# Kernel tuning notes

Measured on AMD Instinct MI355X. Metric: run time of the kernel, lower is better.

## Reference

```python
import jax, jax.numpy as jnp
import numpy as np

V, D = 100000, 300          # vocab, embedding dim
B, L, T, C, I = 64, 256, 1, 10, 6  # batch, positions, targets, context, info samples


def setup_inputs() -> dict:
    key = jax.random.key(0)
    ks = jax.random.split(key, 8)
    # indices start at 1 so padding_idx=0 (zero row, no grad in torch) never appears
    pos_u = jax.random.randint(ks[0], (B, L, T), 1, V)
    pos_v = jax.random.randint(ks[1], (B, L, C), 1, V)
    info_v = jax.random.randint(ks[2], (B, L, I), 1, V)
    initrange = 1.0 / D
    W_out = jax.random.uniform(ks[3], (V, D), minval=-initrange, maxval=initrange, dtype=jnp.float32)
    # torch inits W_in to 0; use a small random init so the baseline is non-degenerate
    W_in = jax.random.uniform(ks[4], (V, D), minval=-initrange, maxval=initrange, dtype=jnp.float32)
    W_out = W_out.at[0].set(0.0)
    W_in = W_in.at[0].set(0.0)
    context_mask = (jax.random.uniform(ks[5], (C,)) > 0.2).astype(jnp.float32)
    sig_mask = jnp.where(jax.random.uniform(ks[6], (I,)) > 0.5, 1.0, -1.0).astype(jnp.float32)
    score_mask = jax.random.uniform(ks[7], (I,), dtype=jnp.float32)
    return {"pos_u": pos_u, "pos_v": pos_v, "info_v": info_v,
            "W_in": W_in, "W_out": W_out,
            "context_mask": context_mask, "sig_mask": sig_mask, "score_mask": score_mask}


def reference(pos_u, pos_v, info_v, W_in, W_out, context_mask, sig_mask, score_mask):
    tgt_out = W_out[pos_u]    # [B,L,T,D]
    ctx_in = W_in[pos_v]      # [B,L,C,D]
    ctx_out = W_out[pos_v]    # [B,L,C,D]
    info_in = W_in[info_v]    # [B,L,I,D]
    # dropout disabled (p=0, eval-mode determinism)
    ctx_in = ctx_in * context_mask[None, None, :, None]
    # target-context scores: [B,L,T,C]
    score = jnp.einsum('bltd,blcd->bltc', tgt_out, ctx_in)
    score = jnp.clip(score, -10.0, 10.0)
    loss = -jnp.sum(jax.nn.log_sigmoid(score))
    # context-info scores: [B,L,C,I]
    info_score = jnp.einsum('blcd,blid->blci', ctx_out, info_in)
    info_score = jnp.clip(info_score, -10.0, 10.0)
    info_score = info_score * sig_mask          # sign flip for negative samples
    info_score = -jax.nn.log_sigmoid(info_score) * score_mask
    return loss + jnp.sum(info_score)
```

## Files before the change

### kernel.cpp

```cpp
#include <hip/hip_runtime.h>

#define D_ 300
#define C_ 10
#define I_ 6
#define NPOS 16384
#define PPB 4
#define NBLK (NPOS / PPB)
#define NDOT 70
#define RED_LD 71

__device__ __forceinline__ float neg_log_sigmoid(float x) {
    return __logf(1.0f + __expf(-x));
}

__device__ __forceinline__ float dot4(float4 a, float4 b) {
    return a.x * b.x + a.y * b.y + a.z * b.z + a.w * b.w;
}

__global__ __launch_bounds__(256, 4) void hg2vec_pos_kernel(
    const int* __restrict__ pos_u, const int* __restrict__ pos_v,
    const int* __restrict__ info_v,
    const float* __restrict__ W_in, const float* __restrict__ W_out,
    const float* __restrict__ context_mask, const float* __restrict__ sig_mask,
    const float* __restrict__ score_mask, float* __restrict__ partial)
{
    const int wave = threadIdx.x >> 6;
    const int lane = threadIdx.x & 63;
    const int p = blockIdx.x * PPB + wave;

    __shared__ float s_red[PPB][8][RED_LD];

    const int su = __builtin_amdgcn_readfirstlane(pos_u[p]);
    int scv[C_], siv[I_];
#pragma unroll
    for (int c = 0; c < C_; ++c) scv[c] = __builtin_amdgcn_readfirstlane(pos_v[p * C_ + c]);
#pragma unroll
    for (int i = 0; i < I_; ++i) siv[i] = __builtin_amdgcn_readfirstlane(info_v[p * I_ + i]);

    const int o0 = 4 * lane;
    const int l1 = (lane < 11) ? lane : 0;
    const int o1 = 256 + 4 * l1;
    const float zf = (lane < 11) ? 1.0f : 0.0f;

    const float* ur = W_out + (size_t)su * D_;
    float4 u0 = *(const float4*)(ur + o0);
    float4 u1 = *(const float4*)(ur + o1);
    u1.x *= zf; u1.y *= zf; u1.z *= zf; u1.w *= zf;

    float4 in0[I_], in1[I_];
#pragma unroll
    for (int i = 0; i < I_; ++i) {
        const float* r = W_in + (size_t)siv[i] * D_;
        in0[i] = *(const float4*)(r + o0);
        float4 t = *(const float4*)(r + o1);
        t.x *= zf; t.y *= zf; t.z *= zf; t.w *= zf;
        in1[i] = t;
    }

    const int g = lane >> 3;
    const bool writer = (lane & 7) == 0;

#pragma unroll
    for (int c = 0; c < C_; ++c) {
        const float* cir = W_in  + (size_t)scv[c] * D_;
        const float* cor = W_out + (size_t)scv[c] * D_;
        const float4 a0 = *(const float4*)(cir + o0);
        const float4 a1 = *(const float4*)(cir + o1);
        const float4 b0 = *(const float4*)(cor + o0);
        const float4 b1 = *(const float4*)(cor + o1);

        float part[7];
        part[0] = dot4(u0, a0) + dot4(u1, a1);
#pragma unroll
        for (int i = 0; i < I_; ++i)
            part[1 + i] = dot4(b0, in0[i]) + dot4(b1, in1[i]);

#pragma unroll
        for (int t = 0; t < 7; ++t) {
            float v = part[t];
            v += __shfl_xor(v, 1, 64);
            v += __shfl_xor(v, 2, 64);
            v += __shfl_xor(v, 4, 64);
            if (writer) s_red[wave][g][c * 7 + t] = v;
        }
    }

    float acc = 0.0f;
#pragma unroll
    for (int pass = 0; pass < 2; ++pass) {
        const int d = pass * 64 + lane;
        if (d < NDOT) {
            float s = s_red[wave][0][d] + s_red[wave][1][d] + s_red[wave][2][d]
                    + s_red[wave][3][d] + s_red[wave][4][d] + s_red[wave][5][d]
                    + s_red[wave][6][d] + s_red[wave][7][d];
            const int c = d / 7;
            const int t = d - c * 7;
            if (t == 0) {
                float x = s * context_mask[c];
                x = fminf(fmaxf(x, -10.0f), 10.0f);
                acc += neg_log_sigmoid(x);
            } else {
                const int i = t - 1;
                float x = fminf(fmaxf(s, -10.0f), 10.0f) * sig_mask[i];
                acc += neg_log_sigmoid(x) * score_mask[i];
            }
        }
    }

#pragma unroll
    for (int off = 32; off; off >>= 1) acc += __shfl_xor(acc, off, 64);
    if (lane == 0) partial[p] = acc;
}

__global__ __launch_bounds__(256) void hg2vec_reduce_kernel(
    const float* __restrict__ partial, float* __restrict__ out)
{
    float a = 0.0f;
    const float4* p4 = (const float4*)partial;
    for (int i = threadIdx.x; i < NPOS / 4; i += 256) {
        float4 v = p4[i];
        a += (v.x + v.y) + (v.z + v.w);
    }
#pragma unroll
    for (int off = 32; off; off >>= 1) a += __shfl_xor(a, off, 64);
    __shared__ float s[4];
    if ((threadIdx.x & 63) == 0) s[threadIdx.x >> 6] = a;
    __syncthreads();
    if (threadIdx.x == 0) out[0] = (s[0] + s[1]) + (s[2] + s[3]);
}

extern "C" void kernel_launch(void* const* d_in, const int* in_sizes, int n_in,
                              void* d_out, int out_size, void* d_ws, size_t ws_size,
                              hipStream_t stream) {
    const int* pos_u = (const int*)d_in[0];
    const int* pos_v = (const int*)d_in[1];
    const int* info_v = (const int*)d_in[2];
    const float* W_in = (const float*)d_in[3];
    const float* W_out = (const float*)d_in[4];
    const float* context_mask = (const float*)d_in[5];
    const float* sig_mask = (const float*)d_in[6];
    const float* score_mask = (const float*)d_in[7];
    float* out = (float*)d_out;
    float* partial = (float*)d_ws;

    hg2vec_pos_kernel<<<NBLK, 256, 0, stream>>>(
        pos_u, pos_v, info_v, W_in, W_out,
        context_mask, sig_mask, score_mask, partial);
    hg2vec_reduce_kernel<<<1, 256, 0, stream>>>(partial, out);
}
```

Baseline: 300.9 us.

## Double-buffer gathered embedding rows into LDS with async global_load_lds per wave

```diff
diff --git a/kernel.cpp b/kernel.cpp
--- a/kernel.cpp
+++ b/kernel.cpp
@@ -4,129 +4,176 @@
 #define C_ 10
 #define I_ 6
 #define NPOS 16384
-#define PPB 4
-#define NBLK (NPOS / PPB)
+#define NROWS 27
 #define NDOT 70
-#define RED_LD 71
+#define ROWF 304
+#define BUFPAD 212
+#define BUFF (NROWS * ROWF + BUFPAD)
+#define WPB 2
+#define PPW 32
+#define NBLK (NPOS / (WPB * PPW))
+#define NPART (NBLK * WPB)
 
 __device__ __forceinline__ float neg_log_sigmoid(float x) {
     return __logf(1.0f + __expf(-x));
 }
-
 __device__ __forceinline__ float dot4(float4 a, float4 b) {
     return a.x * b.x + a.y * b.y + a.z * b.z + a.w * b.w;
 }
+__device__ __forceinline__ void dma16(const float* g, float* l) {
+    __builtin_amdgcn_global_load_lds(
+        (const __attribute__((address_space(1))) void*)g,
+        (__attribute__((address_space(3))) void*)l, 16, 0, 0);
+}
 
-__global__ __launch_bounds__(256, 4) void hg2vec_pos_kernel(
+__global__ __launch_bounds__(128) void hg2vec_pos_kernel(
     const int* __restrict__ pos_u, const int* __restrict__ pos_v,
     const int* __restrict__ info_v,
     const float* __restrict__ W_in, const float* __restrict__ W_out,
     const float* __restrict__ context_mask, const float* __restrict__ sig_mask,
     const float* __restrict__ score_mask, float* __restrict__ partial)
 {
-    const int wave = threadIdx.x >> 6;
+    const int wv = __builtin_amdgcn_readfirstlane((int)(threadIdx.x >> 6));
     const int lane = threadIdx.x & 63;
-    const int p = blockIdx.x * PPB + wave;
+    const int p0 = (blockIdx.x * WPB + wv) * PPW;
 
-    __shared__ float s_red[PPB][8][RED_LD];
+    __shared__ float s_buf[WPB][2][BUFF];
+    __shared__ float s_red[WPB][8][71];
 
-    const int su = __builtin_amdgcn_readfirstlane(pos_u[p]);
-    int scv[C_], siv[I_];
-#pragma unroll
-    for (int c = 0; c < C_; ++c) scv[c] = __builtin_amdgcn_readfirstlane(pos_v[p * C_ + c]);
-#pragma unroll
-    for (int i = 0; i < I_; ++i) siv[i] = __builtin_amdgcn_readfirstlane(info_v[p * I_ + i]);
+    const int d1 = lane;
+    const int c1 = d1 / 7, t1 = d1 - 7 * c1;
+    float m1_cm = 0, m1_sm = 0, m1_scm = 0;
+    if (t1 == 0) m1_cm = context_mask[c1];
+    else { m1_sm = sig_mask[t1 - 1]; m1_scm = score_mask[t1 - 1]; }
+    const int d2 = 64 + lane;
+    const bool has2 = d2 < NDOT;
+    const int c2 = d2 / 7, t2 = d2 - 7 * c2;
+    float m2_sm = 0, m2_scm = 0;
+    if (has2) { m2_sm = sig_mask[t2 - 1]; m2_scm = score_mask[t2 - 1]; }
 
-    const int o0 = 4 * lane;
-    const int l1 = (lane < 11) ? lane : 0;
-    const int o1 = 256 + 4 * l1;
+    const int lc = (lane < 11) ? lane : 10;
     const float zf = (lane < 11) ? 1.0f : 0.0f;
 
-    const float* ur = W_out + (size_t)su * D_;
-    float4 u0 = *(const float4*)(ur + o0);
-    float4 u1 = *(const float4*)(ur + o1);
-    u1.x *= zf; u1.y *= zf; u1.z *= zf; u1.w *= zf;
-
-    float4 in0[I_], in1[I_];
+    int su, scv[C_], siv[I_];
+    auto load_idx = [&](int p) {
+        su = pos_u[p];
 #pragma unroll
-    for (int i = 0; i < I_; ++i) {
-        const float* r = W_in + (size_t)siv[i] * D_;
-        in0[i] = *(const float4*)(r + o0);
-        float4 t = *(const float4*)(r + o1);
-        t.x *= zf; t.y *= zf; t.z *= zf; t.w *= zf;
-        in1[i] = t;
-    }
-
-    const int g = lane >> 3;
-    const bool writer = (lane & 7) == 0;
-
+        for (int c = 0; c < C_; ++c) scv[c] = pos_v[p * C_ + c];
 #pragma unroll
-    for (int c = 0; c < C_; ++c) {
-        const float* cir = W_in  + (size_t)scv[c] * D_;
-        const float* cor = W_out + (size_t)scv[c] * D_;
-        const float4 a0 = *(const float4*)(cir + o0);
-        const float4 a1 = *(const float4*)(cir + o1);
-        const float4 b0 = *(const float4*)(cor + o0);
-        const float4 b1 = *(const float4*)(cor + o1);
-
-        float part[7];
-        part[0] = dot4(u0, a0) + dot4(u1, a1);
+        for (int i = 0; i < I_; ++i) siv[i] = info_v[p * I_ + i];
+    };
+    auto row_g = [&](int r) -> const float* {
+        if (r == 0)  return W_out + (size_t)su * D_;
+        if (r <= 10) return W_in  + (size_t)scv[r - 1] * D_;
+        if (r <= 20) return W_out + (size_t)scv[r - 11] * D_;
+        return W_in + (size_t)siv[r - 21] * D_;
+    };
+    auto fill = [&](int bi) {
+        float* base = &s_buf[wv][bi][0];
 #pragma unroll
-        for (int i = 0; i < I_; ++i)
-            part[1 + i] = dot4(b0, in0[i]) + dot4(b1, in1[i]);
-
+        for (int r = 0; r < NROWS; ++r) {
+            const float* g = row_g(r);
+            if (lane < 11) dma16(g + 256 + 4 * lc, base + r * ROWF + 256);
+        }
 #pragma unroll
-        for (int t = 0; t < 7; ++t) {
-            float v = part[t];
-            v += __shfl_xor(v, 1, 64);
-            v += __shfl_xor(v, 2, 64);
-            v += __shfl_xor(v, 4, 64);
-            if (writer) s_red[wave][g][c * 7 + t] = v;
-        }
-    }
+        for (int r = 0; r < NROWS; ++r)
+            dma16(row_g(r) + 4 * lane, base + r * ROWF);
+    };
 
     float acc = 0.0f;
+
+    load_idx(p0);
+    fill(0);
+
+    for (int j = 0; j < PPW; ++j) {
+        if (j < PPW - 1) {
+            load_idx(p0 + j + 1);
+            fill((j + 1) & 1);
+            asm volatile("s_waitcnt vmcnt(54)" ::: "memory");
+        } else {
+            asm volatile("s_waitcnt vmcnt(0)" ::: "memory");
+        }
+
+        const float* base = &s_buf[wv][j & 1][0];
+        const int o0 = 4 * lane;
+        const int o1 = 256 + 4 * lc;
+
+        float4 u0 = *(const float4*)(base + 0 * ROWF + o0);
+        float4 u1 = *(const float4*)(base + 0 * ROWF + o1);
+        u1.x *= zf; u1.y *= zf; u1.z *= zf; u1.w *= zf;
+        float4 in0[I_], in1[I_];
 #pragma unroll
-    for (int pass = 0; pass < 2; ++pass) {
-        const int d = pass * 64 + lane;
-        if (d < NDOT) {
-            float s = s_red[wave][0][d] + s_red[wave][1][d] + s_red[wave][2][d]
-                    + s_red[wave][3][d] + s_red[wave][4][d] + s_red[wave][5][d]
-                    + s_red[wave][6][d] + s_red[wave][7][d];
-            const int c = d / 7;
-            const int t = d - c * 7;
-            if (t == 0) {
-                float x = s * context_mask[c];
+        for (int i = 0; i < I_; ++i) {
+            const float* r = base + (21 + i) * ROWF;
+            in0[i] = *(const float4*)(r + o0);
+            float4 t = *(const float4*)(r + o1);
+            t.x *= zf; t.y *= zf; t.z *= zf; t.w *= zf;
+            in1[i] = t;
+        }
+
+        const int g = lane >> 3;
+        const bool writer = (lane & 7) == 0;
+#pragma unroll
+        for (int c = 0; c < C_; ++c) {
+            const float* ra = base + (1 + c) * ROWF;
+            const float* rb = base + (11 + c) * ROWF;
+            const float4 a0 = *(const float4*)(ra + o0);
+            const float4 a1 = *(const float4*)(ra + o1);
+            const float4 b0 = *(const float4*)(rb + o0);
+            const float4 b1 = *(const float4*)(rb + o1);
+            float part[7];
+            part[0] = dot4(u0, a0) + dot4(u1, a1);
+#pragma unroll
+            for (int i = 0; i < I_; ++i)
+                part[1 + i] = dot4(b0, in0[i]) + dot4(b1, in1[i]);
+#pragma unroll
+            for (int t = 0; t < 7; ++t) {
+                float v = part[t];
+                v += __shfl_xor(v, 1, 64);
+                v += __shfl_xor(v, 2, 64);
+                v += __shfl_xor(v, 4, 64);
+                if (writer) s_red[wv][g][c * 7 + t] = v;
+            }
+        }
+
+        {
+            float s = s_red[wv][0][d1] + s_red[wv][1][d1] + s_red[wv][2][d1]
+                    + s_red[wv][3][d1] + s_red[wv][4][d1] + s_red[wv][5][d1]
+                    + s_red[wv][6][d1] + s_red[wv][7][d1];
+            if (t1 == 0) {
+                float x = s * m1_cm;
                 x = fminf(fmaxf(x, -10.0f), 10.0f);
                 acc += neg_log_sigmoid(x);
             } else {
-                const int i = t - 1;
-                float x = fminf(fmaxf(s, -10.0f), 10.0f) * sig_mask[i];
-                acc += neg_log_sigmoid(x) * score_mask[i];
+                float x = fminf(fmaxf(s, -10.0f), 10.0f) * m1_sm;
+                acc += neg_log_sigmoid(x) * m1_scm;
+            }
+            if (has2) {
+                float s2 = s_red[wv][0][d2] + s_red[wv][1][d2] + s_red[wv][2][d2]
+                         + s_red[wv][3][d2] + s_red[wv][4][d2] + s_red[wv][5][d2]
+                         + s_red[wv][6][d2] + s_red[wv][7][d2];
+                float x = fminf(fmaxf(s2, -10.0f), 10.0f) * m2_sm;
+                acc += neg_log_sigmoid(x) * m2_scm;
             }
         }
     }
 
 #pragma unroll
     for (int off = 32; off; off >>= 1) acc += __shfl_xor(acc, off, 64);
-    if (lane == 0) partial[p] = acc;
+    if (lane == 0) partial[blockIdx.x * WPB + wv] = acc;
 }
 
-__global__ __launch_bounds__(256) void hg2vec_reduce_kernel(
+__global__ __launch_bounds__(128) void hg2vec_reduce_kernel(
     const float* __restrict__ partial, float* __restrict__ out)
 {
-    float a = 0.0f;
-    const float4* p4 = (const float4*)partial;
-    for (int i = threadIdx.x; i < NPOS / 4; i += 256) {
-        float4 v = p4[i];
-        a += (v.x + v.y) + (v.z + v.w);
-    }
+    float4 v = ((const float4*)partial)[threadIdx.x];
+    float a = (v.x + v.y) + (v.z + v.w);
 #pragma unroll
     for (int off = 32; off; off >>= 1) a += __shfl_xor(a, off, 64);
-    __shared__ float s[4];
+    __shared__ float s[2];
     if ((threadIdx.x & 63) == 0) s[threadIdx.x >> 6] = a;
     __syncthreads();
-    if (threadIdx.x == 0) out[0] = (s[0] + s[1]) + (s[2] + s[3]);
+    if (threadIdx.x == 0) out[0] = s[0] + s[1];
 }
 
 extern "C" void kernel_launch(void* const* d_in, const int* in_sizes, int n_in,
@@ -143,8 +190,8 @@
     float* out = (float*)d_out;
     float* partial = (float*)d_ws;
 
-    hg2vec_pos_kernel<<<NBLK, 256, 0, stream>>>(
+    hg2vec_pos_kernel<<<NBLK, 128, 0, stream>>>(
         pos_u, pos_v, info_v, W_in, W_out,
         context_mask, sig_mask, score_mask, partial);
-    hg2vec_reduce_kernel<<<1, 256, 0, stream>>>(partial, out);
+    hg2vec_reduce_kernel<<<1, 128, 0, stream>>>(partial, out);
 }
```

Measured after the change: 570.0 us. +89.4%, slower.
